# Performance work log

Measured on AMD Instinct MI355X. Metric: run time of the kernel, lower is better.

The kernel has to match this reference:

```python
import jax, jax.numpy as jnp
import numpy as np

D_MODEL = 1024
N_HEADS = 16
D_EXP = 4
B, SQ, SKV = 2, 2048, 2048
LN_EPS = 1e-5


def _linear_params(key, d_in, d_out):
    kw, kb = jax.random.split(key)
    w = jax.random.normal(kw, (d_in, d_out), jnp.float32) * 0.02  # stored [in,out]
    b = jax.random.normal(kb, (d_out,), jnp.float32) * 0.02
    return w, b


def setup_inputs() -> dict:
    key = jax.random.key(0)
    ks = jax.random.split(key, 16)
    inp = {}
    inp["x"] = jax.random.normal(ks[0], (B, SQ, D_MODEL), jnp.float32)
    inp["encoder_out"] = jax.random.normal(ks[1], (B, SKV, D_MODEL), jnp.float32)
    # causal target mask, broadcast over batch and heads
    inp["tgt_mask"] = jnp.tril(jnp.ones((SQ, SQ), jnp.int32))[None, None]
    inp["src_mask"] = jnp.ones((1, 1, SQ, SKV), jnp.int32)
    # self-attention params
    inp["wq_s"], inp["bq_s"] = _linear_params(ks[2], D_MODEL, D_MODEL)
    inp["wk_s"], inp["bk_s"] = _linear_params(ks[3], D_MODEL, D_MODEL)
    inp["wv_s"], inp["bv_s"] = _linear_params(ks[4], D_MODEL, D_MODEL)
    inp["wo_s"], inp["bo_s"] = _linear_params(ks[5], D_MODEL, D_MODEL)
    # cross-attention params
    inp["wq_c"], inp["bq_c"] = _linear_params(ks[6], D_MODEL, D_MODEL)
    inp["wk_c"], inp["bk_c"] = _linear_params(ks[7], D_MODEL, D_MODEL)
    inp["wv_c"], inp["bv_c"] = _linear_params(ks[8], D_MODEL, D_MODEL)
    inp["wo_c"], inp["bo_c"] = _linear_params(ks[9], D_MODEL, D_MODEL)
    # feedforward params
    inp["ff1_w"], inp["ff1_b"] = _linear_params(ks[10], D_MODEL, D_MODEL * D_EXP)
    inp["ff2_w"], inp["ff2_b"] = _linear_params(ks[11], D_MODEL * D_EXP, D_MODEL)
    # layernorm params (3 AddNorms)
    for i, k in zip((1, 2, 3), (ks[12], ks[13], ks[14])):
        inp[f"ln{i}_g"] = jnp.ones((D_MODEL,), jnp.float32)
        inp[f"ln{i}_b"] = jnp.zeros((D_MODEL,), jnp.float32)
    return inp


def _layernorm(x, g, b):
    mu = jnp.mean(x, axis=-1, keepdims=True)
    var = jnp.mean(jnp.square(x - mu), axis=-1, keepdims=True)
    return (x - mu) / jnp.sqrt(var + LN_EPS) * g + b


def _mha(xq, xkv, wq, bq, wk, bk, wv, bv, wo, bo, mask):
    Bq, Sq, D = xq.shape
    Hd = D // N_HEADS
    q = (xq @ wq + bq).reshape(Bq, Sq, N_HEADS, Hd).transpose(0, 2, 1, 3)   # bhqd
    k = (xkv @ wk + bk).reshape(Bq, -1, N_HEADS, Hd).transpose(0, 2, 1, 3)  # bhkd
    v = (xkv @ wv + bv).reshape(Bq, -1, N_HEADS, Hd).transpose(0, 2, 1, 3)  # bhkd
    score = jnp.einsum("bhqd,bhkd->bhqk", q, k) / jnp.sqrt(jnp.float32(Hd))
    score = jnp.where(mask == 0, -jnp.inf, score)
    attn = jax.nn.softmax(score, axis=-1)
    ctx = jnp.einsum("bhqk,bhkd->bhqd", attn, v)
    ctx = ctx.transpose(0, 2, 1, 3).reshape(Bq, Sq, D)
    return ctx @ wo + bo


def reference(x, encoder_out, tgt_mask, src_mask,
              wq_s, bq_s, wk_s, bk_s, wv_s, bv_s, wo_s, bo_s,
              wq_c, bq_c, wk_c, bk_c, wv_c, bv_c, wo_c, bo_c,
              ff1_w, ff1_b, ff2_w, ff2_b,
              ln1_g, ln1_b, ln2_g, ln2_b, ln3_g, ln3_b):
    # dropout is identity in eval mode
    sa = _mha(x, x, wq_s, bq_s, wk_s, bk_s, wv_s, bv_s, wo_s, bo_s, tgt_mask)
    h = _layernorm(x + sa, ln1_g, ln1_b)
    ca = _mha(h, encoder_out, wq_c, bq_c, wk_c, bk_c, wv_c, bv_c, wo_c, bo_c, src_mask)
    h2 = _layernorm(h + ca, ln2_g, ln2_b)
    ff = jax.nn.relu(h2 @ ff1_w + ff1_b) @ ff2_w + ff2_b
    return _layernorm(h2 + ff, ln3_g, ln3_b)
```

## Files before the change

### kernel.cpp

```cpp
#include <hip/hip_runtime.h>
#include <stdint.h>

typedef __bf16 bf16;
typedef __attribute__((ext_vector_type(4))) float f32x4;
typedef __attribute__((ext_vector_type(8))) __bf16 bf16x8;
typedef __attribute__((ext_vector_type(4))) __bf16 bf16x4;

#define DM   1024
#define NH   16
#define HDIM 64
#define BB   2
#define SEQ  2048
#define MR   (BB * SEQ)
#define DFF  4096
#define MEG  (1024 * 1024)

__global__ void detect_kernel(const unsigned int* __restrict__ xw,
                              int* __restrict__ flag) {
  int tid = threadIdx.x;
  int bad = 0;
  for (int i = tid; i < 4096; i += 64) {
    unsigned int w = xw[i];
    float flo = __uint_as_float((w & 0xffffu) << 16);
    if (!(fabsf(flo) < 100.f)) bad = 1;
  }
  unsigned long long m = __ballot(bad);
  if (tid == 0) *flag = (m == 0ull) ? 1 : 0;
}

__global__ __launch_bounds__(256) void cvt_big_kernel(
    const void* __restrict__ src, bf16* __restrict__ dst, int n4,
    const int* __restrict__ flag) {
  int i = blockIdx.x * 256 + threadIdx.x;
  if (i >= n4) return;
  if (*flag) {
    ((bf16x4*)dst)[i] = ((const bf16x4*)src)[i];
  } else {
    float4 v = ((const float4*)src)[i];
    bf16x4 o = {(bf16)v.x, (bf16)v.y, (bf16)v.z, (bf16)v.w};
    ((bf16x4*)dst)[i] = o;
  }
}

struct P16 { const void* p[16]; };
__global__ __launch_bounds__(256) void cvt_small_kernel(
    P16 ps, bf16* __restrict__ dstbase, const int* __restrict__ flag) {
  const int ncnt[16] = {1024,1024,1024,1024,1024,1024,1024,1024,
                        4096,1024,1024,1024,1024,1024,1024,1024};
  const int doff[16] = {0,1024,2048,3072,4096,5120,6144,7168,
                        8192,12288,13312,14336,15360,16384,17408,18432};
  int b = blockIdx.x;
  int n = ncnt[b];
  bool isbf = (*flag) != 0;
  const void* s = ps.p[b];
  bf16* d = dstbase + doff[b];
  for (int i = threadIdx.x; i * 4 < n; i += 256) {
    if (isbf) {
      ((bf16x4*)d)[i] = ((const bf16x4*)s)[i];
    } else {
      float4 v = ((const float4*)s)[i];
      bf16x4 o = {(bf16)v.x, (bf16)v.y, (bf16)v.z, (bf16)v.w};
      ((bf16x4*)d)[i] = o;
    }
  }
}

static __device__ __forceinline__ void gl_lds16(const bf16* g, bf16* l) {
  auto gp = reinterpret_cast<__attribute__((address_space(1))) unsigned int*>(
      reinterpret_cast<uintptr_t>(g));
  auto lp = reinterpret_cast<__attribute__((address_space(3))) unsigned int*>(
      (unsigned int)reinterpret_cast<uintptr_t>(l));
  __builtin_amdgcn_global_load_lds(gp, lp, 16, 0, 0);
}

struct WTB {
  const void* src[10];
  int dstoff[10];
  int K[10], N[10];
  int bstart[10];
};
__global__ __launch_bounds__(256) void wt_all_kernel(WTB wb, bf16* __restrict__ wtbase,
                                                     const int* __restrict__ flag) {
  __shared__ bf16 tile[32][33];
  int bid = blockIdx.x;
  int wi = 0;
  while (wi < 9 && bid >= wb.bstart[wi + 1]) ++wi;
  int rel = bid - wb.bstart[wi];
  int N = wb.N[wi], K = wb.K[wi];
  int nb = N >> 5;
  int n0 = (rel % nb) * 32, k0 = (rel / nb) * 32;
  const void* w = wb.src[wi];
  bf16* wt = wtbase + wb.dstoff[wi];
  bool isbf = (*flag) != 0;
  int tid = threadIdx.x;
  int tx = tid & 31, ty = tid >> 5;
#pragma unroll
  for (int i = 0; i < 4; ++i) {
    size_t idx = (size_t)(k0 + ty + i * 8) * N + n0 + tx;
    tile[ty + i * 8][tx] = isbf ? ((const bf16*)w)[idx]
                                : (bf16)(((const float*)w)[idx]);
  }
  __syncthreads();
#pragma unroll
  for (int i = 0; i < 4; ++i)
    wt[(size_t)(n0 + ty + i * 8) * K + k0 + tx] = tile[tx][ty + i * 8];
}

template <int TM>
__global__ __launch_bounds__(256) void gemm_kernel(
    const bf16* __restrict__ A, const bf16* __restrict__ Bt,
    const bf16* __restrict__ bias, bf16* __restrict__ outb,
    int M, int N, int K, int relu) {
  constexpr int NI = TM / 32;
  constexpr int WM = TM / 2;
  constexpr int CA = TM / 64;
  __shared__ alignas(16) bf16 As[TM * 32];
  __shared__ alignas(16) bf16 Bs[128 * 32];
  int tid = threadIdx.x;
  int lane = tid & 63, wv = tid >> 6;
  int quad = lane >> 4, l15 = lane & 15;
  int m0 = blockIdx.y * TM, n0 = blockIdx.x * 128;
  int wm = wv >> 1, wn = wv & 1;

  f32x4 acc[NI][4];
#pragma unroll
  for (int i = 0; i < NI; ++i)
#pragma unroll
    for (int j = 0; j < 4; ++j) acc[i][j] = (f32x4){0.f, 0.f, 0.f, 0.f};

  int sr = lane >> 2, sc = (lane & 3) * 8;
  const bf16* gA[CA];
  bf16* lA[CA];
#pragma unroll
  for (int t = 0; t < CA; ++t) {
    int ch = wv * CA + t;
    gA[t] = A + (size_t)(m0 + ch * 16 + sr) * K + sc;
    lA[t] = As + ch * 512 + lane * 8;
  }
  const bf16* gB0 = Bt + (size_t)(n0 + (wv * 2) * 16 + sr) * K + sc;
  const bf16* gB1 = Bt + (size_t)(n0 + (wv * 2 + 1) * 16 + sr) * K + sc;
  bf16* lB0 = Bs + (wv * 2) * 512 + lane * 8;
  bf16* lB1 = Bs + (wv * 2 + 1) * 512 + lane * 8;

  for (int k0 = 0; k0 < K; k0 += 32) {
#pragma unroll
    for (int t = 0; t < CA; ++t) gl_lds16(gA[t] + k0, lA[t]);
    gl_lds16(gB0 + k0, lB0);
    gl_lds16(gB1 + k0, lB1);
    __syncthreads();
    bf16x8 af[NI], bfr[4];
#pragma unroll
    for (int i = 0; i < NI; ++i)
      af[i] = *(const bf16x8*)(As + (wm * WM + i * 16 + l15) * 32 + quad * 8);
#pragma unroll
    for (int j = 0; j < 4; ++j)
      bfr[j] = *(const bf16x8*)(Bs + (wn * 64 + j * 16 + l15) * 32 + quad * 8);
#pragma unroll
    for (int i = 0; i < NI; ++i)
#pragma unroll
      for (int j = 0; j < 4; ++j)
        acc[i][j] = __builtin_amdgcn_mfma_f32_16x16x32_bf16(af[i], bfr[j],
                                                            acc[i][j], 0, 0, 0);
    __syncthreads();
  }

#pragma unroll
  for (int j = 0; j < 4; ++j) {
    int col = n0 + wn * 64 + j * 16 + l15;
    float bval = (float)bias[col];
#pragma unroll
    for (int i = 0; i < NI; ++i) {
      int rb = m0 + wm * WM + i * 16 + quad * 4;
#pragma unroll
      for (int r = 0; r < 4; ++r) {
        float v = acc[i][j][r] + bval;
        if (relu) v = fmaxf(v, 0.f);
        outb[(size_t)(rb + r) * N + col] = (bf16)v;
      }
    }
  }
}

__global__ __launch_bounds__(256) void gemm_splitk_kernel(
    const bf16* __restrict__ A, const bf16* __restrict__ Bt,
    float* __restrict__ pout, int M, int N, int KC, int Ktot) {
  __shared__ alignas(16) bf16 As[128 * 32];
  __shared__ alignas(16) bf16 Bs[128 * 32];
  int tid = threadIdx.x;
  int lane = tid & 63, wv = tid >> 6;
  int quad = lane >> 4, l15 = lane & 15;
  int m0 = blockIdx.y * 128, n0 = blockIdx.x * 128;
  int wm = wv >> 1, wn = wv & 1;
  int kb = blockIdx.z * KC;
  pout += (size_t)blockIdx.z * M * N;

  f32x4 acc[4][4];
#pragma unroll
  for (int i = 0; i < 4; ++i)
#pragma unroll
    for (int j = 0; j < 4; ++j) acc[i][j] = (f32x4){0.f, 0.f, 0.f, 0.f};

  int sr = lane >> 2, sc = (lane & 3) * 8;
  const bf16* gA0 = A + (size_t)(m0 + (wv * 2) * 16 + sr) * Ktot + sc;
  const bf16* gA1 = A + (size_t)(m0 + (wv * 2 + 1) * 16 + sr) * Ktot + sc;
  const bf16* gB0 = Bt + (size_t)(n0 + (wv * 2) * 16 + sr) * Ktot + sc;
  const bf16* gB1 = Bt + (size_t)(n0 + (wv * 2 + 1) * 16 + sr) * Ktot + sc;
  bf16* lA0 = As + (wv * 2) * 512 + lane * 8;
  bf16* lA1 = As + (wv * 2 + 1) * 512 + lane * 8;
  bf16* lB0 = Bs + (wv * 2) * 512 + lane * 8;
  bf16* lB1 = Bs + (wv * 2 + 1) * 512 + lane * 8;

  for (int k0 = kb; k0 < kb + KC; k0 += 32) {
    gl_lds16(gA0 + k0, lA0);
    gl_lds16(gA1 + k0, lA1);
    gl_lds16(gB0 + k0, lB0);
    gl_lds16(gB1 + k0, lB1);
    __syncthreads();
    bf16x8 af[4], bfr[4];
#pragma unroll
    for (int i = 0; i < 4; ++i)
      af[i] = *(const bf16x8*)(As + (wm * 64 + i * 16 + l15) * 32 + quad * 8);
#pragma unroll
    for (int j = 0; j < 4; ++j)
      bfr[j] = *(const bf16x8*)(Bs + (wn * 64 + j * 16 + l15) * 32 + quad * 8);
#pragma unroll
    for (int i = 0; i < 4; ++i)
#pragma unroll
      for (int j = 0; j < 4; ++j)
        acc[i][j] = __builtin_amdgcn_mfma_f32_16x16x32_bf16(af[i], bfr[j],
                                                            acc[i][j], 0, 0, 0);
    __syncthreads();
  }
#pragma unroll
  for (int j = 0; j < 4; ++j) {
    int col = n0 + wn * 64 + j * 16 + l15;
#pragma unroll
    for (int i = 0; i < 4; ++i) {
      int rb = m0 + wm * 64 + i * 16 + quad * 4;
#pragma unroll
      for (int r = 0; r < 4; ++r)
        pout[(size_t)(rb + r) * N + col] = acc[i][j][r];
    }
  }
}

__global__ __launch_bounds__(256) void vt_pre_kernel(
    const bf16* __restrict__ v, int vstride, bf16* __restrict__ vt, int skv) {
  __shared__ bf16 tile[32][33];
  int tid = threadIdx.x;
  int tx = tid & 31, ty = tid >> 5;
  int kv0 = blockIdx.x * 32, d0 = blockIdx.y * 32;
  int bh = blockIdx.z;
  int b = bh >> 4, h = bh & 15;
  const bf16* src = v + (size_t)b * skv * vstride + h * HDIM;
#pragma unroll
  for (int i = 0; i < 4; ++i)
    tile[ty + i * 8][tx] = src[(size_t)(kv0 + ty + i * 8) * vstride + d0 + tx];
  __syncthreads();
  bf16* dst = vt + ((size_t)bh * HDIM + d0) * skv + kv0;
#pragma unroll
  for (int i = 0; i < 4; ++i)
    dst[(size_t)(ty + i * 8) * skv + tx] = tile[tx][ty + i * 8];
}

__global__ __launch_bounds__(256) void flash4_kernel(
    const bf16* __restrict__ Q, int qstride,
    const bf16* __restrict__ Kk, int kstride,
    const bf16* __restrict__ VT, bf16* __restrict__ ctx, int skv, int causal) {
  __shared__ alignas(16) bf16 Kt[2][64 * 72];
  __shared__ alignas(16) bf16 Vt[2][64 * 72];
  __shared__ alignas(16) bf16 Pt[2][4][32 * 72];
  int tid = threadIdx.x;
  int lane = tid & 63, wv = tid >> 6, quad = lane >> 4, l15 = lane & 15;
  int qb = blockIdx.x, h = blockIdx.y, b = blockIdx.z;
  int q0 = qb * 128;
  int qw = q0 + wv * 32;

  bf16x8 qf[2][2];
  const float qsc = 0.125f * 1.44269504f;
#pragma unroll
  for (int a = 0; a < 2; ++a) {
    const bf16* qp = Q + (size_t)(b * SEQ + qw + a * 16 + l15) * qstride + h * HDIM;
    qf[a][0] = *(const bf16x8*)(qp + quad * 8);
    qf[a][1] = *(const bf16x8*)(qp + 32 + quad * 8);
#pragma unroll
    for (int j = 0; j < 8; ++j) {
      qf[a][0][j] = (bf16)((float)qf[a][0][j] * qsc);
      qf[a][1][j] = (bf16)((float)qf[a][1][j] * qsc);
    }
  }
  bf16x8 onesf;
#pragma unroll
  for (int j = 0; j < 8; ++j) onesf[j] = (l15 == 0) ? (bf16)1.0f : (bf16)0.0f;

  f32x4 o[2][4], oL[2];
#pragma unroll
  for (int a = 0; a < 2; ++a) {
    oL[a] = (f32x4){0.f, 0.f, 0.f, 0.f};
#pragma unroll
    for (int j = 0; j < 4; ++j) o[a][j] = (f32x4){0.f, 0.f, 0.f, 0.f};
  }

  int nch = causal ? (q0 + 128) / 64 : skv / 64;
  int srow = tid >> 2, sseg = (tid & 3) * 16;
  const bf16* kg = Kk + (size_t)b * skv * kstride + (size_t)srow * kstride +
                   h * HDIM + sseg;
  const bf16* vg = VT + ((size_t)(b * NH + h) * HDIM + srow) * skv + sseg;

  bf16x8 k0r = *(const bf16x8*)(kg);
  bf16x8 k1r = *(const bf16x8*)(kg + 8);
  bf16x8 v0r = *(const bf16x8*)(vg);
  bf16x8 v1r = *(const bf16x8*)(vg + 8);

  for (int c = 0; c < nch; ++c) {
    int buf = c & 1;
    int kv0 = c * 64;
    *(bf16x8*)(&Kt[buf][srow * 72 + sseg]) = k0r;
    *(bf16x8*)(&Kt[buf][srow * 72 + sseg + 8]) = k1r;
    *(bf16x8*)(&Vt[buf][srow * 72 + sseg]) = v0r;
    *(bf16x8*)(&Vt[buf][srow * 72 + sseg + 8]) = v1r;
    if (c + 1 < nch) {
      const bf16* kn = kg + (size_t)(kv0 + 64) * kstride;
      const bf16* vn = vg + kv0 + 64;
      k0r = *(const bf16x8*)(kn);
      k1r = *(const bf16x8*)(kn + 8);
      v0r = *(const bf16x8*)(vn);
      v1r = *(const bf16x8*)(vn + 8);
    }
    __syncthreads();

    if (!causal || kv0 <= qw + 31) {
      f32x4 s[2][4];
#pragma unroll
      for (int t = 0; t < 4; ++t) {
        bf16x8 kt0 = *(const bf16x8*)(&Kt[buf][(t * 16 + l15) * 72 + quad * 8]);
        bf16x8 kt1 = *(const bf16x8*)(&Kt[buf][(t * 16 + l15) * 72 + 32 + quad * 8]);
#pragma unroll
        for (int a = 0; a < 2; ++a) {
          f32x4 z = (f32x4){0.f, 0.f, 0.f, 0.f};
          z = __builtin_amdgcn_mfma_f32_16x16x32_bf16(kt0, qf[a][0], z, 0, 0, 0);
          z = __builtin_amdgcn_mfma_f32_16x16x32_bf16(kt1, qf[a][1], z, 0, 0, 0);
          s[a][t] = z;
        }
      }
      if (causal && kv0 + 63 > qw) {
#pragma unroll
        for (int a = 0; a < 2; ++a)
#pragma unroll
          for (int t = 0; t < 4; ++t)
#pragma unroll
            for (int r = 0; r < 4; ++r)
              if (kv0 + t * 16 + quad * 4 + r > qw + a * 16 + l15)
                s[a][t][r] = -1e30f;
      }
#pragma unroll
      for (int a = 0; a < 2; ++a)
#pragma unroll
        for (int t = 0; t < 4; ++t) {
          bf16x4 pk;
#pragma unroll
          for (int r = 0; r < 4; ++r)
            pk[r] = (bf16)exp2f(s[a][t][r] - 5.770780f);
          *(bf16x4*)(&Pt[buf][wv][(a * 16 + l15) * 72 + t * 16 + quad * 4]) = pk;
        }
      __asm__ volatile("s_waitcnt lgkmcnt(0)" ::: "memory");
      bf16x8 pf[2][2];
#pragma unroll
      for (int a = 0; a < 2; ++a) {
        pf[a][0] = *(const bf16x8*)(&Pt[buf][wv][(a * 16 + l15) * 72 + quad * 8]);
        pf[a][1] = *(const bf16x8*)(&Pt[buf][wv][(a * 16 + l15) * 72 + 32 + quad * 8]);
        oL[a] = __builtin_amdgcn_mfma_f32_16x16x32_bf16(pf[a][0], onesf, oL[a], 0, 0, 0);
        oL[a] = __builtin_amdgcn_mfma_f32_16x16x32_bf16(pf[a][1], onesf, oL[a], 0, 0, 0);
      }
#pragma unroll
      for (int j = 0; j < 4; ++j) {
        bf16x8 bv0 = *(const bf16x8*)(&Vt[buf][(j * 16 + l15) * 72 + quad * 8]);
        bf16x8 bv1 = *(const bf16x8*)(&Vt[buf][(j * 16 + l15) * 72 + 32 + quad * 8]);
#pragma unroll
        for (int a = 0; a < 2; ++a) {
          o[a][j] = __builtin_amdgcn_mfma_f32_16x16x32_bf16(pf[a][0], bv0, o[a][j], 0, 0, 0);
          o[a][j] = __builtin_amdgcn_mfma_f32_16x16x32_bf16(pf[a][1], bv1, o[a][j], 0, 0, 0);
        }
      }
    }
  }

#pragma unroll
  for (int a = 0; a < 2; ++a)
#pragma unroll
    for (int r = 0; r < 4; ++r) {
      float l = __shfl(oL[a][r], quad * 16, 64);
      float inv = 1.0f / fmaxf(l, 1e-30f);
      bf16* cp = ctx + (size_t)(b * SEQ + qw + a * 16 + quad * 4 + r) * DM + h * HDIM;
#pragma unroll
      for (int j = 0; j < 4; ++j) cp[j * 16 + l15] = (bf16)(o[a][j][r] * inv);
    }
}

template <int NP>
__global__ __launch_bounds__(256) void addnorm_red_kernel(
    const bf16* __restrict__ res, const float* __restrict__ part,
    const bf16* __restrict__ bias, const bf16* __restrict__ g,
    const bf16* __restrict__ be, bf16* __restrict__ yb,
    void* __restrict__ outAny, const int* __restrict__ flag) {
  int row = blockIdx.x, tid = threadIdx.x;
  float a0 = 0.f, a1 = 0.f, a2 = 0.f, a3 = 0.f;
#pragma unroll
  for (int p = 0; p < NP; ++p) {
    float4 v = ((const float4*)(part + (size_t)p * MR * DM + (size_t)row * DM))[tid];
    a0 += v.x; a1 += v.y; a2 += v.z; a3 += v.w;
  }
  bf16x4 bb = ((const bf16x4*)bias)[tid];
  bf16x4 rr = ((const bf16x4*)(res + (size_t)row * DM))[tid];
  float s0 = (float)rr[0] + a0 + (float)bb[0];
  float s1 = (float)rr[1] + a1 + (float)bb[1];
  float s2 = (float)rr[2] + a2 + (float)bb[2];
  float s3 = (float)rr[3] + a3 + (float)bb[3];
  float sum = s0 + s1 + s2 + s3;
  float sq = s0 * s0 + s1 * s1 + s2 * s2 + s3 * s3;
#pragma unroll
  for (int mk = 32; mk >= 1; mk >>= 1) {
    sum += __shfl_xor(sum, mk, 64);
    sq += __shfl_xor(sq, mk, 64);
  }
  __shared__ float red[8];
  int wvi = tid >> 6, lane = tid & 63;
  if (lane == 0) { red[wvi * 2] = sum; red[wvi * 2 + 1] = sq; }
  __syncthreads();
  sum = red[0] + red[2] + red[4] + red[6];
  sq = red[1] + red[3] + red[5] + red[7];
  float mu = sum * (1.0f / DM);
  float var = sq * (1.0f / DM) - mu * mu;
  float rstd = rsqrtf(var + 1e-5f);
  bf16x4 g4 = ((const bf16x4*)g)[tid];
  bf16x4 b4 = ((const bf16x4*)be)[tid];
  float y0 = (s0 - mu) * rstd * (float)g4[0] + (float)b4[0];
  float y1 = (s1 - mu) * rstd * (float)g4[1] + (float)b4[1];
  float y2 = (s2 - mu) * rstd * (float)g4[2] + (float)b4[2];
  float y3 = (s3 - mu) * rstd * (float)g4[3] + (float)b4[3];
  if (yb) {
    bf16x4 ob = {(bf16)y0, (bf16)y1, (bf16)y2, (bf16)y3};
    ((bf16x4*)(yb + (size_t)row * DM))[tid] = ob;
  }
  if (outAny) {
    if (*flag) {
      bf16x4 ob = {(bf16)y0, (bf16)y1, (bf16)y2, (bf16)y3};
      ((bf16x4*)outAny)[(size_t)row * 256 + tid] = ob;
    } else {
      ((float4*)outAny)[(size_t)row * 256 + tid] = make_float4(y0, y1, y2, y3);
    }
  }
}

extern "C" void kernel_launch(void* const* d_in, const int* in_sizes, int n_in,
                              void* d_out, int out_size, void* d_ws, size_t ws_size,
                              hipStream_t stream) {
  (void)in_sizes; (void)n_in; (void)out_size; (void)ws_size;
  const void* x_raw   = d_in[0];
  const void* enc_raw = d_in[1];

  char* ws = (char*)d_ws;
  size_t off = 0;
  auto alloc = [&](size_t bytes) -> void* {
    void* p = ws + off;
    off += (bytes + 255) & ~(size_t)255;
    return p;
  };
  const size_t SB = (size_t)MR * DM;
  int* flag    = (int*)alloc(256);
  bf16* smallb = (bf16*)alloc(20480 * 2);
  bf16* wt   = (bf16*)alloc((size_t)16 * MEG * 2);
  bf16* xb   = (bf16*)alloc(SB * 2);
  bf16* encb = (bf16*)alloc(SB * 2);
  bf16* vtg  = (bf16*)alloc(SB * 2);
  bf16* ctx  = (bf16*)alloc(SB * 2);
  bf16* hb1  = (bf16*)alloc(SB * 2);
  bf16* hb2  = (bf16*)alloc(SB * 2);
  bf16* qkv  = (bf16*)alloc(SB * 3 * 2);
  bf16* kvc  = (bf16*)alloc(SB * 2 * 2);
  float* part = (float*)alloc(SB * 4 * 4);
  bf16* gbuf = qkv;
  bf16* qc   = xb;

  bf16* b_qkvs = smallb + 0;     bf16* b_os  = smallb + 3072;
  bf16* b_qc   = smallb + 4096;  bf16* b_kvc = smallb + 5120;
  bf16* b_oc   = smallb + 7168;  bf16* b_f1  = smallb + 8192;
  bf16* b_f2   = smallb + 12288;
  bf16* l1g = smallb + 13312; bf16* l1b = smallb + 14336;
  bf16* l2g = smallb + 15360; bf16* l2b = smallb + 16384;
  bf16* l3g = smallb + 17408; bf16* l3b = smallb + 18432;

  detect_kernel<<<1, 64, 0, stream>>>((const unsigned int*)x_raw, flag);
  cvt_big_kernel<<<(int)(SB / 1024), 256, 0, stream>>>(x_raw, xb, (int)(SB / 4), flag);
  cvt_big_kernel<<<(int)(SB / 1024), 256, 0, stream>>>(enc_raw, encb, (int)(SB / 4), flag);
  P16 ps;
  ps.p[0] = d_in[5];  ps.p[1] = d_in[7];  ps.p[2] = d_in[9];  ps.p[3] = d_in[11];
  ps.p[4] = d_in[13]; ps.p[5] = d_in[15]; ps.p[6] = d_in[17]; ps.p[7] = d_in[19];
  ps.p[8] = d_in[21]; ps.p[9] = d_in[23];
  ps.p[10] = d_in[24]; ps.p[11] = d_in[25]; ps.p[12] = d_in[26];
  ps.p[13] = d_in[27]; ps.p[14] = d_in[28]; ps.p[15] = d_in[29];
  cvt_small_kernel<<<16, 256, 0, stream>>>(ps, smallb, flag);

  WTB wb;
  const int wsrc[10] = {4, 6, 8, 10, 12, 14, 16, 18, 20, 22};
  for (int i = 0; i < 10; ++i) {
    wb.src[i] = d_in[wsrc[i]];
    wb.K[i] = 1024; wb.N[i] = 1024;
    wb.dstoff[i] = i * MEG;
    wb.bstart[i] = i * 1024;
  }
  wb.N[8] = 4096;
  wb.K[9] = 4096; wb.dstoff[9] = 12 * MEG;
  wb.bstart[9] = 8192 + 4096;
  wt_all_kernel<<<16384, 256, 0, stream>>>(wb, wt, flag);

  gemm_kernel<128><<<dim3(24, 32), 256, 0, stream>>>(xb, wt, b_qkvs, qkv,
                                                     MR, 3072, DM, 0);
  vt_pre_kernel<<<dim3(SEQ / 32, 2, 32), 256, 0, stream>>>(qkv + 2048, 3072, vtg, SEQ);
  flash4_kernel<<<dim3(SEQ / 128, NH, BB), 256, 0, stream>>>(
      qkv, 3072, qkv + 1024, 3072, vtg, ctx, SEQ, 1);
  gemm_splitk_kernel<<<dim3(8, 32, 2), 256, 0, stream>>>(
      ctx, wt + (size_t)3 * MEG, part, MR, DM, 512, DM);
  addnorm_red_kernel<2><<<MR, 256, 0, stream>>>(xb, part, b_os, l1g, l1b,
                                                hb1, nullptr, flag);
  gemm_kernel<64><<<dim3(8, 64), 256, 0, stream>>>(hb1, wt + (size_t)4 * MEG,
                                                   b_qc, qc, MR, DM, DM, 0);
  gemm_kernel<128><<<dim3(16, 32), 256, 0, stream>>>(encb, wt + (size_t)5 * MEG,
                                                     b_kvc, kvc, MR, 2048, DM, 0);
  vt_pre_kernel<<<dim3(SEQ / 32, 2, 32), 256, 0, stream>>>(kvc + 1024, 2048, vtg, SEQ);
  flash4_kernel<<<dim3(SEQ / 128, NH, BB), 256, 0, stream>>>(
      qc, 1024, kvc, 2048, vtg, ctx, SEQ, 0);
  gemm_splitk_kernel<<<dim3(8, 32, 2), 256, 0, stream>>>(
      ctx, wt + (size_t)7 * MEG, part, MR, DM, 512, DM);
  addnorm_red_kernel<2><<<MR, 256, 0, stream>>>(hb1, part, b_oc, l2g, l2b,
                                                hb2, nullptr, flag);
  gemm_kernel<128><<<dim3(32, 32), 256, 0, stream>>>(hb2, wt + (size_t)8 * MEG,
                                                     b_f1, gbuf, MR, DFF, DM, 1);
  gemm_splitk_kernel<<<dim3(8, 32, 4), 256, 0, stream>>>(
      gbuf, wt + (size_t)12 * MEG, part, MR, DM, 1024, DFF);
  addnorm_red_kernel<4><<<MR, 256, 0, stream>>>(hb2, part, b_f2, l3g, l3b,
                                                nullptr, d_out, flag);
}
```

Before: 655.8 us.

## Split causal self-attention KV range across two blocks and combine partials

The causal flash kernel now splits each query block's KV chunk range into two halves run by separate blocks (doubling the grid), writing unnormalized fp32 partial outputs and row sums that a new combine kernel sums and normalizes into bf16 context. This targets poor occupancy and load imbalance of the causal attention grid (only 512 blocks with triangular work). The P staging buffer is shrunk to a single 16-row tile per wave, processed one row group at a time, which cuts LDS use. The fixed softmax offset subtraction is dropped. In exchange it adds an extra launch and fp32 partial traffic through global memory.

```diff
diff --git a/kernel.cpp b/kernel.cpp
--- a/kernel.cpp
+++ b/kernel.cpp
@@ -263,16 +263,21 @@
     dst[(size_t)(ty + i * 8) * skv + tx] = tile[tx][ty + i * 8];
 }
 
-__global__ __launch_bounds__(256) void flash4_kernel(
+__global__ __launch_bounds__(256) void flash5_kernel(
     const bf16* __restrict__ Q, int qstride,
     const bf16* __restrict__ Kk, int kstride,
-    const bf16* __restrict__ VT, bf16* __restrict__ ctx, int skv, int causal) {
+    const bf16* __restrict__ VT, bf16* __restrict__ ctx,
+    float* __restrict__ opart, float* __restrict__ lpart,
+    int skv, int causal, int nsplit) {
   __shared__ alignas(16) bf16 Kt[2][64 * 72];
   __shared__ alignas(16) bf16 Vt[2][64 * 72];
-  __shared__ alignas(16) bf16 Pt[2][4][32 * 72];
+  __shared__ alignas(16) bf16 Pt[4][16 * 72];
   int tid = threadIdx.x;
   int lane = tid & 63, wv = tid >> 6, quad = lane >> 4, l15 = lane & 15;
-  int qb = blockIdx.x, h = blockIdx.y, b = blockIdx.z;
+  int qb = blockIdx.x, h = blockIdx.y;
+  int zz = blockIdx.z;
+  int b = (nsplit == 2) ? (zz >> 1) : zz;
+  int half = (nsplit == 2) ? (zz & 1) : 0;
   int q0 = qb * 128;
   int qw = q0 + wv * 32;
 
@@ -301,25 +306,27 @@
     for (int j = 0; j < 4; ++j) o[a][j] = (f32x4){0.f, 0.f, 0.f, 0.f};
   }
 
-  int nch = causal ? (q0 + 128) / 64 : skv / 64;
+  int nch_tot = causal ? (q0 + 128) / 64 : skv / 64;
+  int c_lo = (half * nch_tot) / nsplit;
+  int c_hi = ((half + 1) * nch_tot) / nsplit;
   int srow = tid >> 2, sseg = (tid & 3) * 16;
   const bf16* kg = Kk + (size_t)b * skv * kstride + (size_t)srow * kstride +
                    h * HDIM + sseg;
   const bf16* vg = VT + ((size_t)(b * NH + h) * HDIM + srow) * skv + sseg;
 
-  bf16x8 k0r = *(const bf16x8*)(kg);
-  bf16x8 k1r = *(const bf16x8*)(kg + 8);
-  bf16x8 v0r = *(const bf16x8*)(vg);
-  bf16x8 v1r = *(const bf16x8*)(vg + 8);
-
-  for (int c = 0; c < nch; ++c) {
-    int buf = c & 1;
+  bf16x8 k0r = *(const bf16x8*)(kg + (size_t)(c_lo * 64) * kstride);
+  bf16x8 k1r = *(const bf16x8*)(kg + (size_t)(c_lo * 64) * kstride + 8);
+  bf16x8 v0r = *(const bf16x8*)(vg + c_lo * 64);
+  bf16x8 v1r = *(const bf16x8*)(vg + c_lo * 64 + 8);
+
+  for (int c = c_lo; c < c_hi; ++c) {
+    int buf = (c - c_lo) & 1;
     int kv0 = c * 64;
     *(bf16x8*)(&Kt[buf][srow * 72 + sseg]) = k0r;
     *(bf16x8*)(&Kt[buf][srow * 72 + sseg + 8]) = k1r;
     *(bf16x8*)(&Vt[buf][srow * 72 + sseg]) = v0r;
     *(bf16x8*)(&Vt[buf][srow * 72 + sseg + 8]) = v1r;
-    if (c + 1 < nch) {
+    if (c + 1 < c_hi) {
       const bf16* kn = kg + (size_t)(kv0 + 64) * kstride;
       const bf16* vn = vg + kv0 + 64;
       k0r = *(const bf16x8*)(kn);
@@ -353,22 +360,23 @@
               if (kv0 + t * 16 + quad * 4 + r > qw + a * 16 + l15)
                 s[a][t][r] = -1e30f;
       }
-#pragma unroll
-      for (int a = 0; a < 2; ++a)
+      bf16x8 pf[2][2];
+#pragma unroll
+      for (int a = 0; a < 2; ++a) {
 #pragma unroll
         for (int t = 0; t < 4; ++t) {
           bf16x4 pk;
 #pragma unroll
-          for (int r = 0; r < 4; ++r)
-            pk[r] = (bf16)exp2f(s[a][t][r] - 5.770780f);
-          *(bf16x4*)(&Pt[buf][wv][(a * 16 + l15) * 72 + t * 16 + quad * 4]) = pk;
+          for (int r = 0; r < 4; ++r) pk[r] = (bf16)exp2f(s[a][t][r]);
+          *(bf16x4*)(&Pt[wv][l15 * 72 + t * 16 + quad * 4]) = pk;
         }
-      __asm__ volatile("s_waitcnt lgkmcnt(0)" ::: "memory");
-      bf16x8 pf[2][2];
+        __asm__ volatile("s_waitcnt lgkmcnt(0)" ::: "memory");
+        pf[a][0] = *(const bf16x8*)(&Pt[wv][l15 * 72 + quad * 8]);
+        pf[a][1] = *(const bf16x8*)(&Pt[wv][l15 * 72 + 32 + quad * 8]);
+        __asm__ volatile("s_waitcnt lgkmcnt(0)" ::: "memory");
+      }
 #pragma unroll
       for (int a = 0; a < 2; ++a) {
-        pf[a][0] = *(const bf16x8*)(&Pt[buf][wv][(a * 16 + l15) * 72 + quad * 8]);
-        pf[a][1] = *(const bf16x8*)(&Pt[buf][wv][(a * 16 + l15) * 72 + 32 + quad * 8]);
         oL[a] = __builtin_amdgcn_mfma_f32_16x16x32_bf16(pf[a][0], onesf, oL[a], 0, 0, 0);
         oL[a] = __builtin_amdgcn_mfma_f32_16x16x32_bf16(pf[a][1], onesf, oL[a], 0, 0, 0);
       }
@@ -385,16 +393,52 @@
     }
   }
 
-#pragma unroll
-  for (int a = 0; a < 2; ++a)
-#pragma unroll
-    for (int r = 0; r < 4; ++r) {
-      float l = __shfl(oL[a][r], quad * 16, 64);
-      float inv = 1.0f / fmaxf(l, 1e-30f);
-      bf16* cp = ctx + (size_t)(b * SEQ + qw + a * 16 + quad * 4 + r) * DM + h * HDIM;
-#pragma unroll
-      for (int j = 0; j < 4; ++j) cp[j * 16 + l15] = (bf16)(o[a][j][r] * inv);
-    }
+  if (nsplit == 1) {
+#pragma unroll
+    for (int a = 0; a < 2; ++a)
+#pragma unroll
+      for (int r = 0; r < 4; ++r) {
+        float l = __shfl(oL[a][r], quad * 16, 64);
+        float inv = 1.0f / fmaxf(l, 1e-30f);
+        bf16* cp = ctx + (size_t)(b * SEQ + qw + a * 16 + quad * 4 + r) * DM + h * HDIM;
+#pragma unroll
+        for (int j = 0; j < 4; ++j) cp[j * 16 + l15] = (bf16)(o[a][j][r] * inv);
+      }
+  } else {
+    float* op = opart + (size_t)half * MR * DM;
+#pragma unroll
+    for (int a = 0; a < 2; ++a)
+#pragma unroll
+      for (int r = 0; r < 4; ++r) {
+        float* cp = op + (size_t)(b * SEQ + qw + a * 16 + quad * 4 + r) * DM + h * HDIM;
+#pragma unroll
+        for (int j = 0; j < 4; ++j) cp[j * 16 + l15] = o[a][j][r];
+      }
+    if (l15 == 0) {
+#pragma unroll
+      for (int a = 0; a < 2; ++a)
+#pragma unroll
+        for (int r = 0; r < 4; ++r)
+          lpart[(size_t)((half * BB + b) * NH + h) * SEQ + qw + a * 16 + quad * 4 + r] =
+              oL[a][r];
+    }
+  }
+}
+
+__global__ __launch_bounds__(256) void flash_comb_kernel(
+    const float* __restrict__ opart, const float* __restrict__ lpart,
+    bf16* __restrict__ ctx) {
+  int row = blockIdx.x, tid = threadIdx.x;
+  int b = row >> 11, q = row & (SEQ - 1);
+  int h = tid >> 4;
+  float l = lpart[(size_t)(b * NH + h) * SEQ + q] +
+            lpart[(size_t)((BB + b) * NH + h) * SEQ + q];
+  float inv = 1.0f / fmaxf(l, 1e-30f);
+  f32x4 o0 = ((const f32x4*)(opart + (size_t)row * DM))[tid];
+  f32x4 o1 = ((const f32x4*)(opart + (size_t)MR * DM + (size_t)row * DM))[tid];
+  bf16x4 ob = {(bf16)((o0[0] + o1[0]) * inv), (bf16)((o0[1] + o1[1]) * inv),
+               (bf16)((o0[2] + o1[2]) * inv), (bf16)((o0[3] + o1[3]) * inv)};
+  ((bf16x4*)(ctx + (size_t)row * DM))[tid] = ob;
 }
 
 template <int NP>
@@ -479,6 +523,7 @@
   bf16* qkv  = (bf16*)alloc(SB * 3 * 2);
   bf16* kvc  = (bf16*)alloc(SB * 2 * 2);
   float* part = (float*)alloc(SB * 4 * 4);
+  float* lpart = (float*)alloc((size_t)2 * BB * NH * SEQ * 4);
   bf16* gbuf = qkv;
   bf16* qc   = xb;
 
@@ -517,8 +562,9 @@
   gemm_kernel<128><<<dim3(24, 32), 256, 0, stream>>>(xb, wt, b_qkvs, qkv,
                                                      MR, 3072, DM, 0);
   vt_pre_kernel<<<dim3(SEQ / 32, 2, 32), 256, 0, stream>>>(qkv + 2048, 3072, vtg, SEQ);
-  flash4_kernel<<<dim3(SEQ / 128, NH, BB), 256, 0, stream>>>(
-      qkv, 3072, qkv + 1024, 3072, vtg, ctx, SEQ, 1);
+  flash5_kernel<<<dim3(SEQ / 128, NH, BB * 2), 256, 0, stream>>>(
+      qkv, 3072, qkv + 1024, 3072, vtg, ctx, part, lpart, SEQ, 1, 2);
+  flash_comb_kernel<<<MR, 256, 0, stream>>>(part, lpart, ctx);
   gemm_splitk_kernel<<<dim3(8, 32, 2), 256, 0, stream>>>(
       ctx, wt + (size_t)3 * MEG, part, MR, DM, 512, DM);
   addnorm_red_kernel<2><<<MR, 256, 0, stream>>>(xb, part, b_os, l1g, l1b,
@@ -528,8 +574,8 @@
   gemm_kernel<128><<<dim3(16, 32), 256, 0, stream>>>(encb, wt + (size_t)5 * MEG,
                                                      b_kvc, kvc, MR, 2048, DM, 0);
   vt_pre_kernel<<<dim3(SEQ / 32, 2, 32), 256, 0, stream>>>(kvc + 1024, 2048, vtg, SEQ);
-  flash4_kernel<<<dim3(SEQ / 128, NH, BB), 256, 0, stream>>>(
-      qc, 1024, kvc, 2048, vtg, ctx, SEQ, 0);
+  flash5_kernel<<<dim3(SEQ / 128, NH, BB), 256, 0, stream>>>(
+      qc, 1024, kvc, 2048, vtg, ctx, nullptr, nullptr, SEQ, 0, 1);
   gemm_splitk_kernel<<<dim3(8, 32, 2), 256, 0, stream>>>(
       ctx, wt + (size_t)7 * MEG, part, MR, DM, 512, DM);
   addnorm_red_kernel<2><<<MR, 256, 0, stream>>>(hb1, part, b_oc, l2g, l2b,
```

After: 659.5 us. About the same (+0.6%).
